# Performance work log

Measured on AMD Instinct MI355X. Metric: run time of the kernel, lower is better.

The kernel has to match this reference:

```python
import jax, jax.numpy as jnp
import numpy as np

N, INPUT_DIM, DIM, K, M_BOOK = 8192, 256, 128, 8192, 8
EPS = 1e-5  # torch BatchNorm1d default eps


def _bn(h, g, b, rm, rv):
    # eval-mode BatchNorm1d with running stats (dropout is identity in eval)
    return (h - rm) / jnp.sqrt(rv + EPS) * g + b


def setup_inputs() -> dict:
    key = jax.random.key(0)
    ks = jax.random.split(key, 20)
    s = 0.02
    inp = {
        "x": jax.random.normal(ks[0], (N, INPUT_DIM), jnp.float32),
        # encoder: input_dim -> 128 -> 256 -> dim
        "W1": jax.random.normal(ks[1], (INPUT_DIM, 128), jnp.float32) * s,
        "b1": jnp.zeros((128,), jnp.float32),
        "g1": jnp.ones((128,), jnp.float32),
        "be1": jnp.zeros((128,), jnp.float32),
        "rm1": jax.random.normal(ks[2], (128,), jnp.float32) * 0.1,
        "rv1": jax.random.uniform(ks[3], (128,), jnp.float32, 0.5, 1.5),
        "W2": jax.random.normal(ks[4], (128, 256), jnp.float32) * s,
        "b2": jnp.zeros((256,), jnp.float32),
        "g2": jnp.ones((256,), jnp.float32),
        "be2": jnp.zeros((256,), jnp.float32),
        "rm2": jax.random.normal(ks[5], (256,), jnp.float32) * 0.1,
        "rv2": jax.random.uniform(ks[6], (256,), jnp.float32, 0.5, 1.5),
        "W3": jax.random.normal(ks[7], (256, DIM), jnp.float32) * s,
        "b3": jnp.zeros((DIM,), jnp.float32),
        # m_book codebooks, torch init uniform(-1/K, 1/K)
        "codebooks": jax.random.uniform(ks[8], (M_BOOK, K, DIM), jnp.float32, -1.0 / K, 1.0 / K),
        # decoder: dim -> 256 -> 128 -> input_dim
        "W4": jax.random.normal(ks[9], (DIM, 256), jnp.float32) * s,
        "b4": jnp.zeros((256,), jnp.float32),
        "g3": jnp.ones((256,), jnp.float32),
        "be3": jnp.zeros((256,), jnp.float32),
        "rm3": jax.random.normal(ks[10], (256,), jnp.float32) * 0.1,
        "rv3": jax.random.uniform(ks[11], (256,), jnp.float32, 0.5, 1.5),
        "W5": jax.random.normal(ks[12], (256, 128), jnp.float32) * s,
        "b5": jnp.zeros((128,), jnp.float32),
        "g4": jnp.ones((128,), jnp.float32),
        "be4": jnp.zeros((128,), jnp.float32),
        "rm4": jax.random.normal(ks[13], (128,), jnp.float32) * 0.1,
        "rv4": jax.random.uniform(ks[14], (128,), jnp.float32, 0.5, 1.5),
        "W6": jax.random.normal(ks[15], (128, INPUT_DIM), jnp.float32) * s,
        "b6": jnp.zeros((INPUT_DIM,), jnp.float32),
    }
    return inp


def reference(x, W1, b1, g1, be1, rm1, rv1, W2, b2, g2, be2, rm2, rv2, W3, b3,
              codebooks, W4, b4, g3, be3, rm3, rv3, W5, b5, g4, be4, rm4, rv4, W6, b6):
    # encoder
    h = jax.nn.relu(_bn(x @ W1 + b1, g1, be1, rm1, rv1))
    h = jax.nn.relu(_bn(h @ W2 + b2, g2, be2, rm2, rv2))
    ze = h @ W3 + b3  # [N, DIM]

    # residual VQ over m_book codebooks
    def step(res, E):  # res [N, C], E [K, C]
        # squared distance ||e - r||^2 = ||r||^2 - 2 r.e + ||e||^2 (no [N,K,C] broadcast)
        d = (jnp.sum(res * res, axis=1, keepdims=True)
             - 2.0 * (res @ E.T)
             + jnp.sum(E * E, axis=1)[None, :])  # [N, K]
        idx = jnp.argmin(d, axis=1)  # [N]
        ce = E[idx]  # [N, C]
        return res - ce, (res, ce)

    _, (res_s, ce_s) = jax.lax.scan(step, ze, codebooks)  # each [M_BOOK, N, DIM]
    zq = jnp.sum(ce_s, axis=0)  # [N, DIM]

    # straight-through estimator
    di = ze + jax.lax.stop_gradient(zq - ze)

    # decoder
    h = jax.nn.relu(_bn(di @ W4 + b4, g3, be3, rm3, rv3))
    h = jax.nn.relu(_bn(h @ W5 + b5, g4, be4, rm4, rv4))
    x_hat = h @ W6 + b6  # [N, INPUT_DIM]
    return x_hat, res_s, ce_s
```

## Files before the change

### kernel.cpp

```cpp
#include <hip/hip_runtime.h>
#include <hip/hip_bf16.h>


typedef __bf16 bf16x8 __attribute__((ext_vector_type(8)));
typedef float  f32x4  __attribute__((ext_vector_type(4)));
typedef unsigned short ushort8v __attribute__((ext_vector_type(8)));

#define MFMA16(a,b,c) __builtin_amdgcn_mfma_f32_16x16x32_bf16((a),(b),(c),0,0,0)

__device__ __forceinline__ float b2f(ushort u){ return __uint_as_float(((unsigned)u) << 16); }
__device__ __forceinline__ ushort f2b_rne(float x){
  unsigned u = __float_as_uint(x);
  return (ushort)((u + 0x7fffu + ((u >> 16) & 1u)) >> 16);
}

__device__ __forceinline__ void cvt8(const float* p, bf16x8& h8, bf16x8& l8){
  f32x4 v0 = *(const f32x4*)p;
  f32x4 v1 = *(const f32x4*)(p + 4);
  ushort8v uh, ul;
  #pragma unroll
  for (int i = 0; i < 4; i++){
    float a = v0[i]; ushort h = f2b_rne(a); uh[i] = h;     ul[i]     = f2b_rne(a - b2f(h));
    float b = v1[i]; ushort g = f2b_rne(b); uh[i + 4] = g; ul[i + 4] = f2b_rne(b - b2f(g));
  }
  h8 = __builtin_bit_cast(bf16x8, uh);
  l8 = __builtin_bit_cast(bf16x8, ul);
}

template<int KK, int NN, bool HAS_BLO>
__device__ __forceinline__ f32x4 dotct(const bf16x8* ah, const bf16x8* al,
                                       const ushort* __restrict__ Bfh,
                                       const ushort* __restrict__ Bfl,
                                       int ct, int L){
  constexpr int KS = KK / 32, CT = NN / 16;
  f32x4 acc = {0.f, 0.f, 0.f, 0.f};
  #pragma unroll
  for (int ks = 0; ks < KS; ks++){
    int bo = ((ks * CT + ct) * 64 + L) * 8;
    bf16x8 bh = *(const bf16x8*)(Bfh + bo);
    acc = MFMA16(ah[ks], bh, acc);
    acc = MFMA16(al[ks], bh, acc);
    if constexpr (HAS_BLO){
      bf16x8 bl = *(const bf16x8*)(Bfl + bo);
      acc = MFMA16(ah[ks], bl, acc);
    }
  }
  return acc;
}

__device__ __forceinline__ void swz_body(const float* __restrict__ Wm, ushort* __restrict__ Wfh,
                                         ushort* __restrict__ Wfl, int N, int b){
  int gid = b * 256 + threadIdx.x;
  int k = gid / N, n = gid - k * N;
  int kt = k >> 5, kr = k & 31, nt = n >> 4, nr = n & 15;
  int lane = (kr >> 3) * 16 + nr, tt = kr & 7;
  int o = (((kt * (N >> 4)) + nt) * 64 + lane) * 8 + tt;
  float v = Wm[gid];
  ushort h = f2b_rne(v);
  Wfh[o] = h;
  if (Wfl) Wfl[o] = f2b_rne(v - b2f(h));
}

__global__ __launch_bounds__(256) void k_prep(
    const float* __restrict__ W1, const float* __restrict__ W2, const float* __restrict__ W3,
    const float* __restrict__ W4, const float* __restrict__ W5, const float* __restrict__ W6,
    ushort* W1fh, ushort* W1fl, ushort* W2fh, ushort* W2fl, ushort* W3fh, ushort* W3fl,
    ushort* W4fh, ushort* W5fh, ushort* W6fh,
    const float* g1,const float* be1,const float* rm1,const float* rv1,
    const float* g2,const float* be2,const float* rm2,const float* rv2,
    const float* g3,const float* be3,const float* rm3,const float* rv3,
    const float* g4,const float* be4,const float* rm4,const float* rv4,
    float* s1,float* t1,float* s2,float* t2,float* s3,float* t3,float* s4,float* t4)
{
  int b = blockIdx.x;
  if (b < 768){
    if      (b < 128) swz_body(W1, W1fh, W1fl, 128, b);
    else if (b < 256) swz_body(W2, W2fh, W2fl, 256, b - 128);
    else if (b < 384) swz_body(W3, W3fh, W3fl, 128, b - 256);
    else if (b < 512) swz_body(W4, W4fh, nullptr, 256, b - 384);
    else if (b < 640) swz_body(W5, W5fh, nullptr, 128, b - 512);
    else              swz_body(W6, W6fh, nullptr, 256, b - 640);
  } else {
    int t = threadIdx.x;
    if (t < 128){
      float sa = g1[t] / sqrtf(rv1[t] + 1e-5f);
      s1[t] = sa; t1[t] = be1[t] - rm1[t] * sa;
      float sb = g4[t] / sqrtf(rv4[t] + 1e-5f);
      s4[t] = sb; t4[t] = be4[t] - rm4[t] * sb;
    }
    if (t < 256){
      float sa = g2[t] / sqrtf(rv2[t] + 1e-5f);
      s2[t] = sa; t2[t] = be2[t] - rm2[t] * sa;
      float sb = g3[t] / sqrtf(rv3[t] + 1e-5f);
      s3[t] = sb; t3[t] = be3[t] - rm3[t] * sb;
    }
  }
}

__global__ __launch_bounds__(256) void k_encoder(
    const float* __restrict__ x,
    const ushort* __restrict__ W1fh, const ushort* __restrict__ W1fl,
    const ushort* __restrict__ W2fh, const ushort* __restrict__ W2fl,
    const ushort* __restrict__ W3fh, const ushort* __restrict__ W3fl,
    const float* __restrict__ b1, const float* __restrict__ s1, const float* __restrict__ t1,
    const float* __restrict__ b2, const float* __restrict__ s2, const float* __restrict__ t2,
    const float* __restrict__ b3,
    ushort* __restrict__ rhi, float* __restrict__ res)
{
  __shared__ __align__(16) float sA[16 * 260];
  __shared__ __align__(16) float sB[16 * 132];
  int tid = threadIdx.x;
  int wv = tid >> 6, L = tid & 63;
  int qd = L >> 4, c16 = L & 15;
  int row0 = blockIdx.x * 16;

  bf16x8 a1h[8], a1l[8];
  #pragma unroll
  for (int ks = 0; ks < 8; ks++)
    cvt8(x + (row0 + c16) * 256 + ks * 32 + qd * 8, a1h[ks], a1l[ks]);

  #pragma unroll
  for (int u = 0; u < 2; u++){
    int ct = wv * 2 + u;
    f32x4 acc = dotct<256,128,true>(a1h, a1l, W1fh, W1fl, ct, L);
    int col = ct * 16 + c16;
    float bia = b1[col], sc = s1[col], sh = t1[col];
    #pragma unroll
    for (int i = 0; i < 4; i++){
      float v = (acc[i] + bia) * sc + sh;
      sB[(qd * 4 + i) * 132 + col] = fmaxf(v, 0.f);
    }
  }
  __syncthreads();

  bf16x8 a2h[4], a2l[4];
  #pragma unroll
  for (int ks = 0; ks < 4; ks++)
    cvt8(sB + c16 * 132 + ks * 32 + qd * 8, a2h[ks], a2l[ks]);

  #pragma unroll
  for (int u = 0; u < 4; u++){
    int ct = wv * 4 + u;
    f32x4 acc = dotct<128,256,true>(a2h, a2l, W2fh, W2fl, ct, L);
    int col = ct * 16 + c16;
    float bia = b2[col], sc = s2[col], sh = t2[col];
    #pragma unroll
    for (int i = 0; i < 4; i++){
      float v = (acc[i] + bia) * sc + sh;
      sA[(qd * 4 + i) * 260 + col] = fmaxf(v, 0.f);
    }
  }
  __syncthreads();

  bf16x8 a3h[8], a3l[8];
  #pragma unroll
  for (int ks = 0; ks < 8; ks++)
    cvt8(sA + c16 * 260 + ks * 32 + qd * 8, a3h[ks], a3l[ks]);

  #pragma unroll
  for (int u = 0; u < 2; u++){
    int ct = wv * 2 + u;
    f32x4 acc = dotct<256,128,true>(a3h, a3l, W3fh, W3fl, ct, L);
    int col = ct * 16 + c16;
    float bia = b3[col];
    #pragma unroll
    for (int i = 0; i < 4; i++){
      int row = row0 + qd * 4 + i;
      float v = acc[i] + bia;
      int o = row * 128 + col;
      res[o] = v;
      rhi[o] = f2b_rne(v);
    }
  }
}

__global__ __launch_bounds__(256) void k_decoder(
    const ushort* __restrict__ dhi, const ushort* __restrict__ dlo,
    const ushort* __restrict__ W4fh, const ushort* __restrict__ W5fh,
    const ushort* __restrict__ W6fh,
    const float* __restrict__ b4, const float* __restrict__ s3, const float* __restrict__ t3,
    const float* __restrict__ b5, const float* __restrict__ s4, const float* __restrict__ t4,
    const float* __restrict__ b6,
    float* __restrict__ xhat)
{
  __shared__ __align__(16) float sA[16 * 260];
  __shared__ __align__(16) float sB[16 * 132];
  int tid = threadIdx.x;
  int wv = tid >> 6, L = tid & 63;
  int qd = L >> 4, c16 = L & 15;
  int row0 = blockIdx.x * 16;

  bf16x8 a1h[4], a1l[4];
  #pragma unroll
  for (int ks = 0; ks < 4; ks++){
    int off = (row0 + c16) * 128 + ks * 32 + qd * 8;
    a1h[ks] = *(const bf16x8*)(dhi + off);
    a1l[ks] = *(const bf16x8*)(dlo + off);
  }

  #pragma unroll
  for (int u = 0; u < 4; u++){
    int ct = wv * 4 + u;
    f32x4 acc = dotct<128,256,false>(a1h, a1l, W4fh, nullptr, ct, L);
    int col = ct * 16 + c16;
    float bia = b4[col], sc = s3[col], sh = t3[col];
    #pragma unroll
    for (int i = 0; i < 4; i++){
      float v = (acc[i] + bia) * sc + sh;
      sA[(qd * 4 + i) * 260 + col] = fmaxf(v, 0.f);
    }
  }
  __syncthreads();

  bf16x8 a2h[8], a2l[8];
  #pragma unroll
  for (int ks = 0; ks < 8; ks++)
    cvt8(sA + c16 * 260 + ks * 32 + qd * 8, a2h[ks], a2l[ks]);

  #pragma unroll
  for (int u = 0; u < 2; u++){
    int ct = wv * 2 + u;
    f32x4 acc = dotct<256,128,false>(a2h, a2l, W5fh, nullptr, ct, L);
    int col = ct * 16 + c16;
    float bia = b5[col], sc = s4[col], sh = t4[col];
    #pragma unroll
    for (int i = 0; i < 4; i++){
      float v = (acc[i] + bia) * sc + sh;
      sB[(qd * 4 + i) * 132 + col] = fmaxf(v, 0.f);
    }
  }
  __syncthreads();

  bf16x8 a3h[4], a3l[4];
  #pragma unroll
  for (int ks = 0; ks < 4; ks++)
    cvt8(sB + c16 * 132 + ks * 32 + qd * 8, a3h[ks], a3l[ks]);

  #pragma unroll
  for (int u = 0; u < 4; u++){
    int ct = wv * 4 + u;
    f32x4 acc = dotct<128,256,false>(a3h, a3l, W6fh, nullptr, ct, L);
    int col = ct * 16 + c16;
    float bia = b6[col];
    #pragma unroll
    for (int i = 0; i < 4; i++)
      xhat[(row0 + qd * 4 + i) * 256 + col] = acc[i] + bia;
  }
}

__device__ __forceinline__ void ebook_body(const float* __restrict__ Ef, ushort* __restrict__ Eb,
                                           float* __restrict__ hen, int code, int L){
  float2 e2 = *(const float2*)(Ef + code * 128 + L * 2);
  ushort h0 = f2b_rne(e2.x), h1 = f2b_rne(e2.y);
  int d = L * 2;
  int o = ((((code >> 4) * 4 + (d >> 5)) * 4 + ((d >> 3) & 3)) * 16 + (code & 15)) * 8 + (d & 7);
  *(unsigned*)(Eb + o) = (unsigned)h0 | ((unsigned)h1 << 16);
  float eh0 = b2f(h0), eh1 = b2f(h1);
  float s = eh0 * eh0 + eh1 * eh1;
  #pragma unroll
  for (int mask = 1; mask <= 32; mask <<= 1) s += __shfl_xor(s, mask);
  if (L == 0) hen[code] = 0.5f * s;
}

__global__ __launch_bounds__(256) void k_ebook(const float* __restrict__ Ef,
                                               ushort* __restrict__ Eb, float* __restrict__ hen){
  ebook_body(Ef, Eb, hen, blockIdx.x * 4 + (threadIdx.x >> 6), threadIdx.x & 63);
}

__global__ __launch_bounds__(256, 4) void k_vq_argmin(
  const ushort* __restrict__ Rhi,
  const ushort* __restrict__ Eb, const float* __restrict__ hen,
  float* __restrict__ cq, int* __restrict__ cj)
{
  int rb = blockIdx.x & 63, ch = blockIdx.x >> 6;
  int tid = threadIdx.x;
  int wv = tid >> 6, L = tid & 63;
  int qd = L >> 4, c16 = L & 15;
  int row0 = rb * 128 + wv * 32;

  bf16x8 ah[2][4];
  #pragma unroll
  for (int t = 0; t < 2; t++){
    int r = row0 + t * 16 + c16;
    #pragma unroll
    for (int ks = 0; ks < 4; ks++)
      ah[t][ks] = *(const bf16x8*)(Rhi + r * 128 + ks * 32 + qd * 8);
  }
  float best[2][4]; int bj[2][4];
  #pragma unroll
  for (int t = 0; t < 2; t++)
    #pragma unroll
    for (int i = 0; i < 4; i++){ best[t][i] = -3.0e38f; bj[t][i] = 0; }

  const ushort* eb = Eb + (size_t)ch * 65536 + L * 8;
  const float*  hb = hen + ch * 512 + c16;
  int jb = ch * 512 + c16;

  bf16x8 bA0 = *(const bf16x8*)(eb + 0),    bA1 = *(const bf16x8*)(eb + 512),
         bA2 = *(const bf16x8*)(eb + 1024), bA3 = *(const bf16x8*)(eb + 1536);
  bf16x8 bB0 = *(const bf16x8*)(eb + 2048 + 0),    bB1 = *(const bf16x8*)(eb + 2048 + 512),
         bB2 = *(const bf16x8*)(eb + 2048 + 1024), bB3 = *(const bf16x8*)(eb + 2048 + 1536);
  float hA = hb[0], hB = hb[16];

  #pragma unroll 1
  for (int g = 0; g < 32; g += 2){
    f32x4 accA0 = {0.f,0.f,0.f,0.f}, accA1 = {0.f,0.f,0.f,0.f};
    __builtin_amdgcn_s_setprio(1);
    accA0 = MFMA16(ah[0][0], bA0, accA0); accA0 = MFMA16(ah[0][1], bA1, accA0);
    accA0 = MFMA16(ah[0][2], bA2, accA0); accA0 = MFMA16(ah[0][3], bA3, accA0);
    accA1 = MFMA16(ah[1][0], bA0, accA1); accA1 = MFMA16(ah[1][1], bA1, accA1);
    accA1 = MFMA16(ah[1][2], bA2, accA1); accA1 = MFMA16(ah[1][3], bA3, accA1);
    __builtin_amdgcn_s_setprio(0);
    {
      int gp = (g + 2 < 32) ? g + 2 : 30;
      const ushort* ebp = eb + gp * 2048;
      bA0 = *(const bf16x8*)(ebp + 0);    bA1 = *(const bf16x8*)(ebp + 512);
      bA2 = *(const bf16x8*)(ebp + 1024); bA3 = *(const bf16x8*)(ebp + 1536);
      float hA2 = hb[gp * 16];
      int jc = jb + g * 16;
      #pragma unroll
      for (int i = 0; i < 4; i++){
        float q0 = accA0[i] - hA;
        if (q0 > best[0][i]){ best[0][i] = q0; bj[0][i] = jc; }
        float q1 = accA1[i] - hA;
        if (q1 > best[1][i]){ best[1][i] = q1; bj[1][i] = jc; }
      }
      hA = hA2;
    }
    f32x4 accB0 = {0.f,0.f,0.f,0.f}, accB1 = {0.f,0.f,0.f,0.f};
    __builtin_amdgcn_s_setprio(1);
    accB0 = MFMA16(ah[0][0], bB0, accB0); accB0 = MFMA16(ah[0][1], bB1, accB0);
    accB0 = MFMA16(ah[0][2], bB2, accB0); accB0 = MFMA16(ah[0][3], bB3, accB0);
    accB1 = MFMA16(ah[1][0], bB0, accB1); accB1 = MFMA16(ah[1][1], bB1, accB1);
    accB1 = MFMA16(ah[1][2], bB2, accB1); accB1 = MFMA16(ah[1][3], bB3, accB1);
    __builtin_amdgcn_s_setprio(0);
    {
      int gq = (g + 3 < 32) ? g + 3 : 31;
      const ushort* ebq = eb + gq * 2048;
      bB0 = *(const bf16x8*)(ebq + 0);    bB1 = *(const bf16x8*)(ebq + 512);
      bB2 = *(const bf16x8*)(ebq + 1024); bB3 = *(const bf16x8*)(ebq + 1536);
      float hB2 = hb[gq * 16];
      int jc = jb + (g + 1) * 16;
      #pragma unroll
      for (int i = 0; i < 4; i++){
        float q0 = accB0[i] - hB;
        if (q0 > best[0][i]){ best[0][i] = q0; bj[0][i] = jc; }
        float q1 = accB1[i] - hB;
        if (q1 > best[1][i]){ best[1][i] = q1; bj[1][i] = jc; }
      }
      hB = hB2;
    }
  }

  #pragma unroll
  for (int mask = 1; mask <= 8; mask <<= 1){
    #pragma unroll
    for (int t = 0; t < 2; t++)
      #pragma unroll
      for (int i = 0; i < 4; i++){
        float ob = __shfl_xor(best[t][i], mask);
        int   oj = __shfl_xor(bj[t][i], mask);
        if (ob > best[t][i] || (ob == best[t][i] && oj < bj[t][i])){ best[t][i] = ob; bj[t][i] = oj; }
      }
  }
  if (c16 == 0){
    #pragma unroll
    for (int t = 0; t < 2; t++)
      #pragma unroll
      for (int i = 0; i < 4; i++){
        int r = row0 + t * 16 + qd * 4 + i;
        cq[r * 16 + ch] = best[t][i];
        cj[r * 16 + ch] = bj[t][i];
      }
  }
}

template<bool LAST>
__global__ __launch_bounds__(256) void k_vq_update(
  const float* __restrict__ cq, const int* __restrict__ cj,
  const float* __restrict__ Ef, const float* __restrict__ Efn,
  ushort* __restrict__ Eb, float* __restrict__ hen,
  float* __restrict__ res, const float* __restrict__ ze_s,
  ushort* __restrict__ rhi, ushort* __restrict__ rlo,
  float* __restrict__ res_s, float* __restrict__ ce_s)
{
  int idx = blockIdx.x * 4 + (threadIdx.x >> 6);
  int L = threadIdx.x & 63;
  int c = L & 15;
  float bq = cq[idx * 16 + c]; int bi = cj[idx * 16 + c];
  #pragma unroll
  for (int mask = 1; mask <= 8; mask <<= 1){
    float ob = __shfl_xor(bq, mask);
    int   oj = __shfl_xor(bi, mask);
    if (ob > bq || (ob == bq && oj < bi)){ bq = ob; bi = oj; }
  }
  int o = idx * 128 + L * 2;
  float2 ce = *(const float2*)(Ef + bi * 128 + L * 2);
  float2 r2 = *(const float2*)(res + o);
  *(float2*)(res_s + o) = r2;
  *(float2*)(ce_s + o) = ce;
  float rn0 = r2.x - ce.x, rn1 = r2.y - ce.y;
  if constexpr (LAST){
    float2 z2 = *(const float2*)(ze_s + o);
    float d0 = z2.x - rn0, d1 = z2.y - rn1;
    ushort h0 = f2b_rne(d0), h1 = f2b_rne(d1);
    *(unsigned*)(rhi + o) = (unsigned)h0 | ((unsigned)h1 << 16);
    ushort l0 = f2b_rne(d0 - b2f(h0)), l1 = f2b_rne(d1 - b2f(h1));
    *(unsigned*)(rlo + o) = (unsigned)l0 | ((unsigned)l1 << 16);
  } else {
    res[o] = rn0; res[o + 1] = rn1;
    ushort h0 = f2b_rne(rn0), h1 = f2b_rne(rn1);
    *(unsigned*)(rhi + o) = (unsigned)h0 | ((unsigned)h1 << 16);
    ebook_body(Efn, Eb, hen, idx, L);
  }
}

extern "C" void kernel_launch(void* const* d_in, const int* in_sizes, int n_in,
                              void* d_out, int out_size, void* d_ws, size_t ws_size,
                              hipStream_t stream)
{
  const float* x   = (const float*)d_in[0];
  const float* W1  = (const float*)d_in[1];
  const float* b1  = (const float*)d_in[2];
  const float* g1  = (const float*)d_in[3];
  const float* be1 = (const float*)d_in[4];
  const float* rm1 = (const float*)d_in[5];
  const float* rv1 = (const float*)d_in[6];
  const float* W2  = (const float*)d_in[7];
  const float* b2  = (const float*)d_in[8];
  const float* g2  = (const float*)d_in[9];
  const float* be2 = (const float*)d_in[10];
  const float* rm2 = (const float*)d_in[11];
  const float* rv2 = (const float*)d_in[12];
  const float* W3  = (const float*)d_in[13];
  const float* b3  = (const float*)d_in[14];
  const float* CB  = (const float*)d_in[15];
  const float* W4  = (const float*)d_in[16];
  const float* b4  = (const float*)d_in[17];
  const float* g3  = (const float*)d_in[18];
  const float* be3 = (const float*)d_in[19];
  const float* rm3 = (const float*)d_in[20];
  const float* rv3 = (const float*)d_in[21];
  const float* W5  = (const float*)d_in[22];
  const float* b5  = (const float*)d_in[23];
  const float* g4  = (const float*)d_in[24];
  const float* be4 = (const float*)d_in[25];
  const float* rm4 = (const float*)d_in[26];
  const float* rv4 = (const float*)d_in[27];
  const float* W6  = (const float*)d_in[28];
  const float* b6  = (const float*)d_in[29];

  char* w = (char*)d_ws;
  ushort* Eb   = (ushort*)(w + 0);
  float*  cq   = (float*) (w + 2097152);
  int*    cj   = (int*)   (w + 2621440);
  ushort* rhi  = (ushort*)(w + 12582912);
  ushort* rlo  = (ushort*)(w + 14680064);
  float*  res  = (float*) (w + 16777216);
  float*  hen  = (float*) (w + 25165824);
  float*  s1   = (float*) (w + 25198592);
  float*  t1   = (float*) (w + 25199104);
  float*  s2   = (float*) (w + 25199616);
  float*  t2   = (float*) (w + 25200640);
  float*  s3   = (float*) (w + 25201664);
  float*  t3   = (float*) (w + 25202688);
  float*  s4   = (float*) (w + 25203712);
  float*  t4   = (float*) (w + 25204224);
  ushort* W1fh = (ushort*)(w + 25204736);
  ushort* W2fh = (ushort*)(w + 25270272);
  ushort* W3fh = (ushort*)(w + 25335808);
  ushort* W4fh = (ushort*)(w + 25401344);
  ushort* W5fh = (ushort*)(w + 25466880);
  ushort* W6fh = (ushort*)(w + 25532416);
  ushort* W1fl = (ushort*)(w + 25597952);
  ushort* W2fl = (ushort*)(w + 25663488);
  ushort* W3fl = (ushort*)(w + 25729024);

  float* xhat  = (float*)d_out;
  float* res_s = xhat + 2097152;
  float* ce_s  = res_s + 8388608;

  k_prep<<<769, 256, 0, stream>>>(W1, W2, W3, W4, W5, W6,
                                  W1fh, W1fl, W2fh, W2fl, W3fh, W3fl,
                                  W4fh, W5fh, W6fh,
                                  g1,be1,rm1,rv1, g2,be2,rm2,rv2,
                                  g3,be3,rm3,rv3, g4,be4,rm4,rv4,
                                  s1,t1,s2,t2,s3,t3,s4,t4);

  k_encoder<<<512, 256, 0, stream>>>(x, W1fh, W1fl, W2fh, W2fl, W3fh, W3fl,
                                     b1, s1, t1, b2, s2, t2, b3,
                                     rhi, res);

  k_ebook<<<2048, 256, 0, stream>>>(CB, Eb, hen);
  for (int m = 0; m < 8; m++){
    const float* Ef = CB + (size_t)m * 1048576;
    k_vq_argmin<<<1024, 256, 0, stream>>>(rhi, Eb, hen, cq, cj);
    if (m < 7){
      k_vq_update<false><<<2048, 256, 0, stream>>>(cq, cj, Ef, Ef + 1048576, Eb, hen,
                                                   res, nullptr, rhi, nullptr,
                                                   res_s + (size_t)m * 1048576,
                                                   ce_s  + (size_t)m * 1048576);
    } else {
      k_vq_update<true><<<2048, 256, 0, stream>>>(cq, cj, Ef, nullptr, Eb, hen,
                                                  res, res_s , rhi, rlo,
                                                  res_s + (size_t)m * 1048576,
                                                  ce_s  + (size_t)m * 1048576);
    }
  }

  k_decoder<<<512, 256, 0, stream>>>(rhi, rlo, W4fh, W5fh, W6fh,
                                     b4, s3, t3, b5, s4, t4, b6, xhat);
}
```

Before: 445.8 us.

## Enlarge VQ argmin row tile to 128 rows per wave and split codebook 32 ways

The argmin kernel now holds 8 row-tiles (128 rows) of the residual per wave instead of 2, so each loaded codebook fragment feeds 8 MFMAs rather than 2. The codebook is split into 32 chunks of 256 codes instead of 16 of 512, and the grid shrinks from 1024 to 512 blocks. The -||e||^2/2 bias is folded into the accumulator initial value, which removes a subtract per element. The candidate buffers widen to 32 per row and the update kernel's reduction grows to match. The aim is to cut codebook load traffic per MFMA, at the cost of much higher register pressure and lower occupancy (launch bounds 2).

Result: slower. 791.5 us (+77.5%).

```diff
diff --git a/kernel.cpp b/kernel.cpp
--- a/kernel.cpp
+++ b/kernel.cpp
@@ -267,95 +267,98 @@
   ebook_body(Ef, Eb, hen, blockIdx.x * 4 + (threadIdx.x >> 6), threadIdx.x & 63);
 }
 
-__global__ __launch_bounds__(256, 4) void k_vq_argmin(
+__global__ __launch_bounds__(256, 2) void k_vq_argmin(
   const ushort* __restrict__ Rhi,
   const ushort* __restrict__ Eb, const float* __restrict__ hen,
   float* __restrict__ cq, int* __restrict__ cj)
 {
-  int rb = blockIdx.x & 63, ch = blockIdx.x >> 6;
+  int rb = blockIdx.x & 15, ch = blockIdx.x >> 4;
   int tid = threadIdx.x;
   int wv = tid >> 6, L = tid & 63;
   int qd = L >> 4, c16 = L & 15;
-  int row0 = rb * 128 + wv * 32;
-
-  bf16x8 ah[2][4];
-  #pragma unroll
-  for (int t = 0; t < 2; t++){
+  int row0 = rb * 512 + wv * 128;
+
+  bf16x8 ah[8][4];
+  #pragma unroll
+  for (int t = 0; t < 8; t++){
     int r = row0 + t * 16 + c16;
     #pragma unroll
     for (int ks = 0; ks < 4; ks++)
       ah[t][ks] = *(const bf16x8*)(Rhi + r * 128 + ks * 32 + qd * 8);
   }
-  float best[2][4]; int bj[2][4];
-  #pragma unroll
-  for (int t = 0; t < 2; t++)
+  float best[8][4]; int bj[8][4];
+  #pragma unroll
+  for (int t = 0; t < 8; t++)
     #pragma unroll
     for (int i = 0; i < 4; i++){ best[t][i] = -3.0e38f; bj[t][i] = 0; }
 
-  const ushort* eb = Eb + (size_t)ch * 65536 + L * 8;
-  const float*  hb = hen + ch * 512 + c16;
-  int jb = ch * 512 + c16;
-
-  bf16x8 bA0 = *(const bf16x8*)(eb + 0),    bA1 = *(const bf16x8*)(eb + 512),
-         bA2 = *(const bf16x8*)(eb + 1024), bA3 = *(const bf16x8*)(eb + 1536);
-  bf16x8 bB0 = *(const bf16x8*)(eb + 2048 + 0),    bB1 = *(const bf16x8*)(eb + 2048 + 512),
-         bB2 = *(const bf16x8*)(eb + 2048 + 1024), bB3 = *(const bf16x8*)(eb + 2048 + 1536);
+  const ushort* eb = Eb + (size_t)ch * 32768 + L * 8;
+  const float*  hb = hen + ch * 256 + c16;
+  int jb = ch * 256 + c16;
+
+  bf16x8 bA[4], bB[4];
+  #pragma unroll
+  for (int k = 0; k < 4; k++) bA[k] = *(const bf16x8*)(eb + k * 512);
+  #pragma unroll
+  for (int k = 0; k < 4; k++) bB[k] = *(const bf16x8*)(eb + 2048 + k * 512);
   float hA = hb[0], hB = hb[16];
 
   #pragma unroll 1
-  for (int g = 0; g < 32; g += 2){
-    f32x4 accA0 = {0.f,0.f,0.f,0.f}, accA1 = {0.f,0.f,0.f,0.f};
-    __builtin_amdgcn_s_setprio(1);
-    accA0 = MFMA16(ah[0][0], bA0, accA0); accA0 = MFMA16(ah[0][1], bA1, accA0);
-    accA0 = MFMA16(ah[0][2], bA2, accA0); accA0 = MFMA16(ah[0][3], bA3, accA0);
-    accA1 = MFMA16(ah[1][0], bA0, accA1); accA1 = MFMA16(ah[1][1], bA1, accA1);
-    accA1 = MFMA16(ah[1][2], bA2, accA1); accA1 = MFMA16(ah[1][3], bA3, accA1);
-    __builtin_amdgcn_s_setprio(0);
+  for (int g = 0; g < 16; g += 2){
     {
-      int gp = (g + 2 < 32) ? g + 2 : 30;
+      float mh = -hA;
+      f32x4 acc[8];
+      #pragma unroll
+      for (int t = 0; t < 8; t++) acc[t] = (f32x4){mh, mh, mh, mh};
+      __builtin_amdgcn_s_setprio(1);
+      #pragma unroll
+      for (int ks = 0; ks < 4; ks++)
+        #pragma unroll
+        for (int t = 0; t < 8; t++)
+          acc[t] = MFMA16(ah[t][ks], bA[ks], acc[t]);
+      __builtin_amdgcn_s_setprio(0);
+      int gp = (g + 2 < 16) ? g + 2 : 14;
       const ushort* ebp = eb + gp * 2048;
-      bA0 = *(const bf16x8*)(ebp + 0);    bA1 = *(const bf16x8*)(ebp + 512);
-      bA2 = *(const bf16x8*)(ebp + 1024); bA3 = *(const bf16x8*)(ebp + 1536);
-      float hA2 = hb[gp * 16];
+      #pragma unroll
+      for (int k = 0; k < 4; k++) bA[k] = *(const bf16x8*)(ebp + k * 512);
+      hA = hb[gp * 16];
       int jc = jb + g * 16;
       #pragma unroll
-      for (int i = 0; i < 4; i++){
-        float q0 = accA0[i] - hA;
-        if (q0 > best[0][i]){ best[0][i] = q0; bj[0][i] = jc; }
-        float q1 = accA1[i] - hA;
-        if (q1 > best[1][i]){ best[1][i] = q1; bj[1][i] = jc; }
-      }
-      hA = hA2;
-    }
-    f32x4 accB0 = {0.f,0.f,0.f,0.f}, accB1 = {0.f,0.f,0.f,0.f};
-    __builtin_amdgcn_s_setprio(1);
-    accB0 = MFMA16(ah[0][0], bB0, accB0); accB0 = MFMA16(ah[0][1], bB1, accB0);
-    accB0 = MFMA16(ah[0][2], bB2, accB0); accB0 = MFMA16(ah[0][3], bB3, accB0);
-    accB1 = MFMA16(ah[1][0], bB0, accB1); accB1 = MFMA16(ah[1][1], bB1, accB1);
-    accB1 = MFMA16(ah[1][2], bB2, accB1); accB1 = MFMA16(ah[1][3], bB3, accB1);
-    __builtin_amdgcn_s_setprio(0);
+      for (int t = 0; t < 8; t++)
+        #pragma unroll
+        for (int i = 0; i < 4; i++)
+          if (acc[t][i] > best[t][i]){ best[t][i] = acc[t][i]; bj[t][i] = jc; }
+    }
     {
-      int gq = (g + 3 < 32) ? g + 3 : 31;
+      float mh = -hB;
+      f32x4 acc[8];
+      #pragma unroll
+      for (int t = 0; t < 8; t++) acc[t] = (f32x4){mh, mh, mh, mh};
+      __builtin_amdgcn_s_setprio(1);
+      #pragma unroll
+      for (int ks = 0; ks < 4; ks++)
+        #pragma unroll
+        for (int t = 0; t < 8; t++)
+          acc[t] = MFMA16(ah[t][ks], bB[ks], acc[t]);
+      __builtin_amdgcn_s_setprio(0);
+      int gq = (g + 3 < 16) ? g + 3 : 15;
       const ushort* ebq = eb + gq * 2048;
-      bB0 = *(const bf16x8*)(ebq + 0);    bB1 = *(const bf16x8*)(ebq + 512);
-      bB2 = *(const bf16x8*)(ebq + 1024); bB3 = *(const bf16x8*)(ebq + 1536);
-      float hB2 = hb[gq * 16];
+      #pragma unroll
+      for (int k = 0; k < 4; k++) bB[k] = *(const bf16x8*)(ebq + k * 512);
+      hB = hb[gq * 16];
       int jc = jb + (g + 1) * 16;
       #pragma unroll
-      for (int i = 0; i < 4; i++){
-        float q0 = accB0[i] - hB;
-        if (q0 > best[0][i]){ best[0][i] = q0; bj[0][i] = jc; }
-        float q1 = accB1[i] - hB;
-        if (q1 > best[1][i]){ best[1][i] = q1; bj[1][i] = jc; }
-      }
-      hB = hB2;
+      for (int t = 0; t < 8; t++)
+        #pragma unroll
+        for (int i = 0; i < 4; i++)
+          if (acc[t][i] > best[t][i]){ best[t][i] = acc[t][i]; bj[t][i] = jc; }
     }
   }
 
   #pragma unroll
   for (int mask = 1; mask <= 8; mask <<= 1){
     #pragma unroll
-    for (int t = 0; t < 2; t++)
+    for (int t = 0; t < 8; t++)
       #pragma unroll
       for (int i = 0; i < 4; i++){
         float ob = __shfl_xor(best[t][i], mask);
@@ -365,12 +368,12 @@
   }
   if (c16 == 0){
     #pragma unroll
-    for (int t = 0; t < 2; t++)
+    for (int t = 0; t < 8; t++)
       #pragma unroll
       for (int i = 0; i < 4; i++){
         int r = row0 + t * 16 + qd * 4 + i;
-        cq[r * 16 + ch] = best[t][i];
-        cj[r * 16 + ch] = bj[t][i];
+        cq[r * 32 + ch] = best[t][i];
+        cj[r * 32 + ch] = bj[t][i];
       }
   }
 }
@@ -386,10 +389,10 @@
 {
   int idx = blockIdx.x * 4 + (threadIdx.x >> 6);
   int L = threadIdx.x & 63;
-  int c = L & 15;
-  float bq = cq[idx * 16 + c]; int bi = cj[idx * 16 + c];
-  #pragma unroll
-  for (int mask = 1; mask <= 8; mask <<= 1){
+  int c = L & 31;
+  float bq = cq[idx * 32 + c]; int bi = cj[idx * 32 + c];
+  #pragma unroll
+  for (int mask = 1; mask <= 16; mask <<= 1){
     float ob = __shfl_xor(bq, mask);
     int   oj = __shfl_xor(bi, mask);
     if (ob > bq || (ob == bq && oj < bi)){ bq = ob; bi = oj; }
@@ -453,7 +456,7 @@
   char* w = (char*)d_ws;
   ushort* Eb   = (ushort*)(w + 0);
   float*  cq   = (float*) (w + 2097152);
-  int*    cj   = (int*)   (w + 2621440);
+  int*    cj   = (int*)   (w + 3145728);
   ushort* rhi  = (ushort*)(w + 12582912);
   ushort* rlo  = (ushort*)(w + 14680064);
   float*  res  = (float*) (w + 16777216);
@@ -494,7 +497,7 @@
   k_ebook<<<2048, 256, 0, stream>>>(CB, Eb, hen);
   for (int m = 0; m < 8; m++){
     const float* Ef = CB + (size_t)m * 1048576;
-    k_vq_argmin<<<1024, 256, 0, stream>>>(rhi, Eb, hen, cq, cj);
+    k_vq_argmin<<<512, 256, 0, stream>>>(rhi, Eb, hen, cq, cj);
     if (m < 7){
       k_vq_update<false><<<2048, 256, 0, stream>>>(cq, cj, Ef, Ef + 1048576, Eb, hen,
                                                    res, nullptr, rhi, nullptr,
```

## Shrink VQ argmin tile to 16 rows per wave and double the grid

Applied to the files above, without the earlier changes.

The argmin kernel now gives each wave 16 residual rows instead of 32, drops the software-pipelined double-buffered codebook loads and the setprio hints, and folds the codebook norm into the MFMA accumulator init. Launch bounds go from 4 to 8 blocks per SIMD and the grid doubles to 2048 blocks. The goal is more occupancy and fewer registers so other waves hide latency. In exchange each codebook fragment loaded from memory is reused by half as many rows, so codebook traffic doubles, and the explicit prefetch is gone.

After: 539.5 us. 21.0% more time.

```diff
diff --git a/kernel.cpp b/kernel.cpp
--- a/kernel.cpp
+++ b/kernel.cpp
@@ -267,111 +267,66 @@
   ebook_body(Ef, Eb, hen, blockIdx.x * 4 + (threadIdx.x >> 6), threadIdx.x & 63);
 }
 
-__global__ __launch_bounds__(256, 4) void k_vq_argmin(
+__global__ __launch_bounds__(256, 8) void k_vq_argmin(
   const ushort* __restrict__ Rhi,
   const ushort* __restrict__ Eb, const float* __restrict__ hen,
   float* __restrict__ cq, int* __restrict__ cj)
 {
-  int rb = blockIdx.x & 63, ch = blockIdx.x >> 6;
+  int blk = blockIdx.x;
+  int rb = blk & 127, ch = blk >> 7;
   int tid = threadIdx.x;
   int wv = tid >> 6, L = tid & 63;
   int qd = L >> 4, c16 = L & 15;
-  int row0 = rb * 128 + wv * 32;
-
-  bf16x8 ah[2][4];
-  #pragma unroll
-  for (int t = 0; t < 2; t++){
-    int r = row0 + t * 16 + c16;
-    #pragma unroll
-    for (int ks = 0; ks < 4; ks++)
-      ah[t][ks] = *(const bf16x8*)(Rhi + r * 128 + ks * 32 + qd * 8);
-  }
-  float best[2][4]; int bj[2][4];
-  #pragma unroll
-  for (int t = 0; t < 2; t++)
-    #pragma unroll
-    for (int i = 0; i < 4; i++){ best[t][i] = -3.0e38f; bj[t][i] = 0; }
+  int row0 = rb * 64 + wv * 16;
+
+  bf16x8 ah[4];
+  #pragma unroll
+  for (int ks = 0; ks < 4; ks++)
+    ah[ks] = *(const bf16x8*)(Rhi + (row0 + c16) * 128 + ks * 32 + qd * 8);
+
+  float best[4]; int bj[4];
+  #pragma unroll
+  for (int i = 0; i < 4; i++){ best[i] = -3.0e38f; bj[i] = 0; }
 
   const ushort* eb = Eb + (size_t)ch * 65536 + L * 8;
   const float*  hb = hen + ch * 512 + c16;
   int jb = ch * 512 + c16;
 
-  bf16x8 bA0 = *(const bf16x8*)(eb + 0),    bA1 = *(const bf16x8*)(eb + 512),
-         bA2 = *(const bf16x8*)(eb + 1024), bA3 = *(const bf16x8*)(eb + 1536);
-  bf16x8 bB0 = *(const bf16x8*)(eb + 2048 + 0),    bB1 = *(const bf16x8*)(eb + 2048 + 512),
-         bB2 = *(const bf16x8*)(eb + 2048 + 1024), bB3 = *(const bf16x8*)(eb + 2048 + 1536);
-  float hA = hb[0], hB = hb[16];
-
   #pragma unroll 1
-  for (int g = 0; g < 32; g += 2){
-    f32x4 accA0 = {0.f,0.f,0.f,0.f}, accA1 = {0.f,0.f,0.f,0.f};
-    __builtin_amdgcn_s_setprio(1);
-    accA0 = MFMA16(ah[0][0], bA0, accA0); accA0 = MFMA16(ah[0][1], bA1, accA0);
-    accA0 = MFMA16(ah[0][2], bA2, accA0); accA0 = MFMA16(ah[0][3], bA3, accA0);
-    accA1 = MFMA16(ah[1][0], bA0, accA1); accA1 = MFMA16(ah[1][1], bA1, accA1);
-    accA1 = MFMA16(ah[1][2], bA2, accA1); accA1 = MFMA16(ah[1][3], bA3, accA1);
-    __builtin_amdgcn_s_setprio(0);
-    {
-      int gp = (g + 2 < 32) ? g + 2 : 30;
-      const ushort* ebp = eb + gp * 2048;
-      bA0 = *(const bf16x8*)(ebp + 0);    bA1 = *(const bf16x8*)(ebp + 512);
-      bA2 = *(const bf16x8*)(ebp + 1024); bA3 = *(const bf16x8*)(ebp + 1536);
-      float hA2 = hb[gp * 16];
-      int jc = jb + g * 16;
-      #pragma unroll
-      for (int i = 0; i < 4; i++){
-        float q0 = accA0[i] - hA;
-        if (q0 > best[0][i]){ best[0][i] = q0; bj[0][i] = jc; }
-        float q1 = accA1[i] - hA;
-        if (q1 > best[1][i]){ best[1][i] = q1; bj[1][i] = jc; }
-      }
-      hA = hA2;
-    }
-    f32x4 accB0 = {0.f,0.f,0.f,0.f}, accB1 = {0.f,0.f,0.f,0.f};
-    __builtin_amdgcn_s_setprio(1);
-    accB0 = MFMA16(ah[0][0], bB0, accB0); accB0 = MFMA16(ah[0][1], bB1, accB0);
-    accB0 = MFMA16(ah[0][2], bB2, accB0); accB0 = MFMA16(ah[0][3], bB3, accB0);
-    accB1 = MFMA16(ah[1][0], bB0, accB1); accB1 = MFMA16(ah[1][1], bB1, accB1);
-    accB1 = MFMA16(ah[1][2], bB2, accB1); accB1 = MFMA16(ah[1][3], bB3, accB1);
-    __builtin_amdgcn_s_setprio(0);
-    {
-      int gq = (g + 3 < 32) ? g + 3 : 31;
-      const ushort* ebq = eb + gq * 2048;
-      bB0 = *(const bf16x8*)(ebq + 0);    bB1 = *(const bf16x8*)(ebq + 512);
-      bB2 = *(const bf16x8*)(ebq + 1024); bB3 = *(const bf16x8*)(ebq + 1536);
-      float hB2 = hb[gq * 16];
-      int jc = jb + (g + 1) * 16;
-      #pragma unroll
-      for (int i = 0; i < 4; i++){
-        float q0 = accB0[i] - hB;
-        if (q0 > best[0][i]){ best[0][i] = q0; bj[0][i] = jc; }
-        float q1 = accB1[i] - hB;
-        if (q1 > best[1][i]){ best[1][i] = q1; bj[1][i] = jc; }
-      }
-      hB = hB2;
-    }
+  for (int g = 0; g < 32; ++g){
+    const ushort* ebg = eb + g * 2048;
+    bf16x8 b0 = *(const bf16x8*)(ebg + 0);
+    bf16x8 b1 = *(const bf16x8*)(ebg + 512);
+    bf16x8 b2 = *(const bf16x8*)(ebg + 1024);
+    bf16x8 b3 = *(const bf16x8*)(ebg + 1536);
+    float mh = -hb[g * 16];
+    f32x4 acc = {mh, mh, mh, mh};
+    acc = MFMA16(ah[0], b0, acc);
+    acc = MFMA16(ah[1], b1, acc);
+    acc = MFMA16(ah[2], b2, acc);
+    acc = MFMA16(ah[3], b3, acc);
+    int jc = jb + g * 16;
+    #pragma unroll
+    for (int i = 0; i < 4; i++)
+      if (acc[i] > best[i]){ best[i] = acc[i]; bj[i] = jc; }
   }
 
   #pragma unroll
   for (int mask = 1; mask <= 8; mask <<= 1){
     #pragma unroll
-    for (int t = 0; t < 2; t++)
-      #pragma unroll
-      for (int i = 0; i < 4; i++){
-        float ob = __shfl_xor(best[t][i], mask);
-        int   oj = __shfl_xor(bj[t][i], mask);
-        if (ob > best[t][i] || (ob == best[t][i] && oj < bj[t][i])){ best[t][i] = ob; bj[t][i] = oj; }
-      }
+    for (int i = 0; i < 4; i++){
+      float ob = __shfl_xor(best[i], mask);
+      int   oj = __shfl_xor(bj[i], mask);
+      if (ob > best[i] || (ob == best[i] && oj < bj[i])){ best[i] = ob; bj[i] = oj; }
+    }
   }
   if (c16 == 0){
     #pragma unroll
-    for (int t = 0; t < 2; t++)
-      #pragma unroll
-      for (int i = 0; i < 4; i++){
-        int r = row0 + t * 16 + qd * 4 + i;
-        cq[r * 16 + ch] = best[t][i];
-        cj[r * 16 + ch] = bj[t][i];
-      }
+    for (int i = 0; i < 4; i++){
+      int r = row0 + qd * 4 + i;
+      cq[r * 16 + ch] = best[i];
+      cj[r * 16 + ch] = bj[i];
+    }
   }
 }
 
@@ -494,7 +449,7 @@
   k_ebook<<<2048, 256, 0, stream>>>(CB, Eb, hen);
   for (int m = 0; m < 8; m++){
     const float* Ef = CB + (size_t)m * 1048576;
-    k_vq_argmin<<<1024, 256, 0, stream>>>(rhi, Eb, hen, cq, cj);
+    k_vq_argmin<<<2048, 256, 0, stream>>>(rhi, Eb, hen, cq, cj);
     if (m < 7){
       k_vq_update<false><<<2048, 256, 0, stream>>>(cq, cj, Ef, Ef + 1048576, Eb, hen,
                                                    res, nullptr, rhi, nullptr,
```

## Stage codebook tiles through double-buffered LDS in argmin and fold ebook into prep

Applied to the files above, without the earlier changes.

The VQ argmin kernel now loads each 512-code codebook chunk cooperatively into a double-buffered shared-memory tile, with one block barrier per 64-code tile. The next tile is prefetched into registers while the current one is consumed. Before, each wave issued its own global loads with a software-pipelined register prefetch. The half-norm bias is also staged in LDS and folded into the MFMA accumulator's initial value, which removes the per-element subtraction. The first-codebook conversion kernel is merged into the prep launch to save one kernel launch. In exchange, the argmin kernel uses about 34 KB of LDS per block and adds barriers, which may reduce occupancy under its 4-blocks-per-CU launch bound.

Measured after the change: 416.7 us. 1.07x faster.

```diff
diff --git a/kernel.cpp b/kernel.cpp
--- a/kernel.cpp
+++ b/kernel.cpp
@@ -46,6 +46,20 @@
     }
   }
   return acc;
+}
+
+__device__ __forceinline__ void ebook_body(const float* __restrict__ Ef, ushort* __restrict__ Eb,
+                                           float* __restrict__ hen, int code, int L){
+  float2 e2 = *(const float2*)(Ef + code * 128 + L * 2);
+  ushort h0 = f2b_rne(e2.x), h1 = f2b_rne(e2.y);
+  int d = L * 2;
+  int o = ((((code >> 4) * 4 + (d >> 5)) * 4 + ((d >> 3) & 3)) * 16 + (code & 15)) * 8 + (d & 7);
+  *(unsigned*)(Eb + o) = (unsigned)h0 | ((unsigned)h1 << 16);
+  float eh0 = b2f(h0), eh1 = b2f(h1);
+  float s = eh0 * eh0 + eh1 * eh1;
+  #pragma unroll
+  for (int mask = 1; mask <= 32; mask <<= 1) s += __shfl_xor(s, mask);
+  if (L == 0) hen[code] = 0.5f * s;
 }
 
 __device__ __forceinline__ void swz_body(const float* __restrict__ Wm, ushort* __restrict__ Wfh,
@@ -66,6 +80,7 @@
     const float* __restrict__ W4, const float* __restrict__ W5, const float* __restrict__ W6,
     ushort* W1fh, ushort* W1fl, ushort* W2fh, ushort* W2fl, ushort* W3fh, ushort* W3fl,
     ushort* W4fh, ushort* W5fh, ushort* W6fh,
+    const float* __restrict__ CB, ushort* __restrict__ Eb, float* __restrict__ hen,
     const float* g1,const float* be1,const float* rm1,const float* rv1,
     const float* g2,const float* be2,const float* rm2,const float* rv2,
     const float* g3,const float* be3,const float* rm3,const float* rv3,
@@ -80,7 +95,7 @@
     else if (b < 512) swz_body(W4, W4fh, nullptr, 256, b - 384);
     else if (b < 640) swz_body(W5, W5fh, nullptr, 128, b - 512);
     else              swz_body(W6, W6fh, nullptr, 256, b - 640);
-  } else {
+  } else if (b == 768){
     int t = threadIdx.x;
     if (t < 128){
       float sa = g1[t] / sqrtf(rv1[t] + 1e-5f);
@@ -94,6 +109,8 @@
       float sb = g3[t] / sqrtf(rv3[t] + 1e-5f);
       s3[t] = sb; t3[t] = be3[t] - rm3[t] * sb;
     }
+  } else {
+    ebook_body(CB, Eb, hen, (b - 769) * 4 + (threadIdx.x >> 6), threadIdx.x & 63);
   }
 }
 
@@ -248,30 +265,13 @@
   }
 }
 
-__device__ __forceinline__ void ebook_body(const float* __restrict__ Ef, ushort* __restrict__ Eb,
-                                           float* __restrict__ hen, int code, int L){
-  float2 e2 = *(const float2*)(Ef + code * 128 + L * 2);
-  ushort h0 = f2b_rne(e2.x), h1 = f2b_rne(e2.y);
-  int d = L * 2;
-  int o = ((((code >> 4) * 4 + (d >> 5)) * 4 + ((d >> 3) & 3)) * 16 + (code & 15)) * 8 + (d & 7);
-  *(unsigned*)(Eb + o) = (unsigned)h0 | ((unsigned)h1 << 16);
-  float eh0 = b2f(h0), eh1 = b2f(h1);
-  float s = eh0 * eh0 + eh1 * eh1;
-  #pragma unroll
-  for (int mask = 1; mask <= 32; mask <<= 1) s += __shfl_xor(s, mask);
-  if (L == 0) hen[code] = 0.5f * s;
-}
-
-__global__ __launch_bounds__(256) void k_ebook(const float* __restrict__ Ef,
-                                               ushort* __restrict__ Eb, float* __restrict__ hen){
-  ebook_body(Ef, Eb, hen, blockIdx.x * 4 + (threadIdx.x >> 6), threadIdx.x & 63);
-}
-
 __global__ __launch_bounds__(256, 4) void k_vq_argmin(
   const ushort* __restrict__ Rhi,
   const ushort* __restrict__ Eb, const float* __restrict__ hen,
   float* __restrict__ cq, int* __restrict__ cj)
 {
+  __shared__ __align__(16) ushort etile[2][8192];
+  __shared__ float henl[512];
   int rb = blockIdx.x & 63, ch = blockIdx.x >> 6;
   int tid = threadIdx.x;
   int wv = tid >> 6, L = tid & 63;
@@ -286,70 +286,74 @@
     for (int ks = 0; ks < 4; ks++)
       ah[t][ks] = *(const bf16x8*)(Rhi + r * 128 + ks * 32 + qd * 8);
   }
+  henl[tid] = hen[ch * 512 + tid];
+  henl[tid + 256] = hen[ch * 512 + 256 + tid];
+
   float best[2][4]; int bj[2][4];
   #pragma unroll
   for (int t = 0; t < 2; t++)
     #pragma unroll
     for (int i = 0; i < 4; i++){ best[t][i] = -3.0e38f; bj[t][i] = 0; }
 
-  const ushort* eb = Eb + (size_t)ch * 65536 + L * 8;
-  const float*  hb = hen + ch * 512 + c16;
+  const ushort* ebc = Eb + (size_t)ch * 65536;
   int jb = ch * 512 + c16;
 
-  bf16x8 bA0 = *(const bf16x8*)(eb + 0),    bA1 = *(const bf16x8*)(eb + 512),
-         bA2 = *(const bf16x8*)(eb + 1024), bA3 = *(const bf16x8*)(eb + 1536);
-  bf16x8 bB0 = *(const bf16x8*)(eb + 2048 + 0),    bB1 = *(const bf16x8*)(eb + 2048 + 512),
-         bB2 = *(const bf16x8*)(eb + 2048 + 1024), bB3 = *(const bf16x8*)(eb + 2048 + 1536);
-  float hA = hb[0], hB = hb[16];
+  {
+    const ushort* src = ebc + tid * 8;
+    f32x4 v0 = *(const f32x4*)(src + 0 * 2048);
+    f32x4 v1 = *(const f32x4*)(src + 1 * 2048);
+    f32x4 v2 = *(const f32x4*)(src + 2 * 2048);
+    f32x4 v3 = *(const f32x4*)(src + 3 * 2048);
+    *(f32x4*)(etile[0] + 0 * 2048 + tid * 8) = v0;
+    *(f32x4*)(etile[0] + 1 * 2048 + tid * 8) = v1;
+    *(f32x4*)(etile[0] + 2 * 2048 + tid * 8) = v2;
+    *(f32x4*)(etile[0] + 3 * 2048 + tid * 8) = v3;
+  }
+  __syncthreads();
 
   #pragma unroll 1
-  for (int g = 0; g < 32; g += 2){
-    f32x4 accA0 = {0.f,0.f,0.f,0.f}, accA1 = {0.f,0.f,0.f,0.f};
-    __builtin_amdgcn_s_setprio(1);
-    accA0 = MFMA16(ah[0][0], bA0, accA0); accA0 = MFMA16(ah[0][1], bA1, accA0);
-    accA0 = MFMA16(ah[0][2], bA2, accA0); accA0 = MFMA16(ah[0][3], bA3, accA0);
-    accA1 = MFMA16(ah[1][0], bA0, accA1); accA1 = MFMA16(ah[1][1], bA1, accA1);
-    accA1 = MFMA16(ah[1][2], bA2, accA1); accA1 = MFMA16(ah[1][3], bA3, accA1);
-    __builtin_amdgcn_s_setprio(0);
-    {
-      int gp = (g + 2 < 32) ? g + 2 : 30;
-      const ushort* ebp = eb + gp * 2048;
-      bA0 = *(const bf16x8*)(ebp + 0);    bA1 = *(const bf16x8*)(ebp + 512);
-      bA2 = *(const bf16x8*)(ebp + 1024); bA3 = *(const bf16x8*)(ebp + 1536);
-      float hA2 = hb[gp * 16];
-      int jc = jb + g * 16;
+  for (int tile = 0; tile < 8; ++tile){
+    int cur = tile & 1;
+    f32x4 v0, v1, v2, v3;
+    if (tile < 7){
+      const ushort* src = ebc + (tile + 1) * 8192 + tid * 8;
+      v0 = *(const f32x4*)(src + 0 * 2048);
+      v1 = *(const f32x4*)(src + 1 * 2048);
+      v2 = *(const f32x4*)(src + 2 * 2048);
+      v3 = *(const f32x4*)(src + 3 * 2048);
+    }
+    const ushort* lb = etile[cur];
+    #pragma unroll
+    for (int g = 0; g < 4; ++g){
+      const ushort* gp = lb + g * 2048 + L * 8;
+      bf16x8 b0 = *(const bf16x8*)(gp + 0);
+      bf16x8 b1 = *(const bf16x8*)(gp + 512);
+      bf16x8 b2 = *(const bf16x8*)(gp + 1024);
+      bf16x8 b3 = *(const bf16x8*)(gp + 1536);
+      int gg = tile * 4 + g;
+      float mh = -henl[gg * 16 + c16];
+      f32x4 a0 = {mh, mh, mh, mh}, a1 = {mh, mh, mh, mh};
+      __builtin_amdgcn_s_setprio(1);
+      a0 = MFMA16(ah[0][0], b0, a0); a1 = MFMA16(ah[1][0], b0, a1);
+      a0 = MFMA16(ah[0][1], b1, a0); a1 = MFMA16(ah[1][1], b1, a1);
+      a0 = MFMA16(ah[0][2], b2, a0); a1 = MFMA16(ah[1][2], b2, a1);
+      a0 = MFMA16(ah[0][3], b3, a0); a1 = MFMA16(ah[1][3], b3, a1);
+      __builtin_amdgcn_s_setprio(0);
+      int jc = jb + gg * 16;
       #pragma unroll
       for (int i = 0; i < 4; i++){
-        float q0 = accA0[i] - hA;
-        if (q0 > best[0][i]){ best[0][i] = q0; bj[0][i] = jc; }
-        float q1 = accA1[i] - hA;
-        if (q1 > best[1][i]){ best[1][i] = q1; bj[1][i] = jc; }
+        if (a0[i] > best[0][i]){ best[0][i] = a0[i]; bj[0][i] = jc; }
+        if (a1[i] > best[1][i]){ best[1][i] = a1[i]; bj[1][i] = jc; }
       }
-      hA = hA2;
-    }
-    f32x4 accB0 = {0.f,0.f,0.f,0.f}, accB1 = {0.f,0.f,0.f,0.f};
-    __builtin_amdgcn_s_setprio(1);
-    accB0 = MFMA16(ah[0][0], bB0, accB0); accB0 = MFMA16(ah[0][1], bB1, accB0);
-    accB0 = MFMA16(ah[0][2], bB2, accB0); accB0 = MFMA16(ah[0][3], bB3, accB0);
-    accB1 = MFMA16(ah[1][0], bB0, accB1); accB1 = MFMA16(ah[1][1], bB1, accB1);
-    accB1 = MFMA16(ah[1][2], bB2, accB1); accB1 = MFMA16(ah[1][3], bB3, accB1);
-    __builtin_amdgcn_s_setprio(0);
-    {
-      int gq = (g + 3 < 32) ? g + 3 : 31;
-      const ushort* ebq = eb + gq * 2048;
-      bB0 = *(const bf16x8*)(ebq + 0);    bB1 = *(const bf16x8*)(ebq + 512);
-      bB2 = *(const bf16x8*)(ebq + 1024); bB3 = *(const bf16x8*)(ebq + 1536);
-      float hB2 = hb[gq * 16];
-      int jc = jb + (g + 1) * 16;
-      #pragma unroll
-      for (int i = 0; i < 4; i++){
-        float q0 = accB0[i] - hB;
-        if (q0 > best[0][i]){ best[0][i] = q0; bj[0][i] = jc; }
-        float q1 = accB1[i] - hB;
-        if (q1 > best[1][i]){ best[1][i] = q1; bj[1][i] = jc; }
-      }
-      hB = hB2;
-    }
+    }
+    if (tile < 7){
+      ushort* nb = etile[cur ^ 1];
+      *(f32x4*)(nb + 0 * 2048 + tid * 8) = v0;
+      *(f32x4*)(nb + 1 * 2048 + tid * 8) = v1;
+      *(f32x4*)(nb + 2 * 2048 + tid * 8) = v2;
+      *(f32x4*)(nb + 3 * 2048 + tid * 8) = v3;
+    }
+    __syncthreads();
   }
 
   #pragma unroll
@@ -480,18 +484,18 @@
   float* res_s = xhat + 2097152;
   float* ce_s  = res_s + 8388608;
 
-  k_prep<<<769, 256, 0, stream>>>(W1, W2, W3, W4, W5, W6,
-                                  W1fh, W1fl, W2fh, W2fl, W3fh, W3fl,
-                                  W4fh, W5fh, W6fh,
-                                  g1,be1,rm1,rv1, g2,be2,rm2,rv2,
-                                  g3,be3,rm3,rv3, g4,be4,rm4,rv4,
-                                  s1,t1,s2,t2,s3,t3,s4,t4);
+  k_prep<<<2817, 256, 0, stream>>>(W1, W2, W3, W4, W5, W6,
+                                   W1fh, W1fl, W2fh, W2fl, W3fh, W3fl,
+                                   W4fh, W5fh, W6fh,
+                                   CB, Eb, hen,
+                                   g1,be1,rm1,rv1, g2,be2,rm2,rv2,
+                                   g3,be3,rm3,rv3, g4,be4,rm4,rv4,
+                                   s1,t1,s2,t2,s3,t3,s4,t4);
 
   k_encoder<<<512, 256, 0, stream>>>(x, W1fh, W1fl, W2fh, W2fl, W3fh, W3fl,
                                      b1, s1, t1, b2, s2, t2, b3,
                                      rhi, res);
 
-  k_ebook<<<2048, 256, 0, stream>>>(CB, Eb, hen);
   for (int m = 0; m < 8; m++){
     const float* Ef = CB + (size_t)m * 1048576;
     k_vq_argmin<<<1024, 256, 0, stream>>>(rhi, Eb, hen, cq, cj);
```
